# Performance work log

Hardware: AMD Instinct MI355X
Metric: run time of the kernel (lower is better)

Reference implementation:

```python
import jax, jax.numpy as jnp
import numpy as np

B, T, C = 2, 2048, 2048
N_HEAD = 16

def setup_inputs() -> dict:
    key = jax.random.key(0)
    k1, k2, k3 = jax.random.split(key, 3)
    scale = 1.0 / np.sqrt(C)
    return {
        "x": jax.random.normal(k1, (B, T, C), dtype=jnp.float32),
        "w_attn": jax.random.normal(k2, (C, 3 * C), dtype=jnp.float32) * scale,
        "b_attn": jnp.zeros((3 * C,), dtype=jnp.float32),
        "w_proj": jax.random.normal(k3, (C, C), dtype=jnp.float32) * scale,
        "b_proj": jnp.zeros((C,), dtype=jnp.float32),
    }

def reference(x, w_attn, b_attn, w_proj, b_proj):
    Bb, Tt, Cc = x.shape
    hd = Cc // N_HEAD  # head_size
    qkv = x @ w_attn + b_attn              # [B,T,3C]
    q, k, v = jnp.split(qkv, 3, axis=-1)
    # [B,T,C] -> [B,H,T,hd]
    def heads(t):
        return t.reshape(Bb, Tt, N_HEAD, hd).transpose(0, 2, 1, 3)
    q, k, v = heads(q), heads(k), heads(v)
    att = jnp.einsum("bhqd,bhkd->bhqk", q, k) * (hd ** -0.5)
    causal = jnp.tril(jnp.ones((Tt, Tt), dtype=bool))
    att = jnp.where(causal[None, None], att, -jnp.inf)
    att = jax.nn.softmax(att, axis=-1)
    out = jnp.einsum("bhqk,bhkd->bhqd", att, v)
    out = out.transpose(0, 2, 1, 3).reshape(Bb, Tt, Cc)
    return out @ w_proj + b_proj
```

## Files before the change

kernel.cpp:

```cpp
#include <hip/hip_runtime.h>
#include <cstdint>
#include <cstddef>

typedef __bf16 bf16_t;
typedef __bf16 bf16x8 __attribute__((ext_vector_type(8)));
typedef __bf16 bf16x4 __attribute__((ext_vector_type(4)));
typedef float floatx4 __attribute__((ext_vector_type(4)));

#define B_  2
#define T_  2048
#define C_  2048
#define H_  16
#define HD_ 128

#define K_ATTN_SCALE (0.08838834764831843f * 1.44269504088896f)

__device__ __forceinline__ void async_copy16(const void* g, void* l) {
  __builtin_amdgcn_global_load_lds((const __attribute__((address_space(1))) unsigned int*)g,
                                   (__attribute__((address_space(3))) unsigned int*)l,
                                   16, 0, 0);
}

__global__ __launch_bounds__(256) void cvt_f32_bf16(const float* __restrict__ in,
                                                    bf16_t* __restrict__ out, int n4) {
  int i = blockIdx.x * 256 + threadIdx.x;
  if (i >= n4) return;
  const float4 v = ((const float4*)in)[i];
  bf16x4 o;
  o[0] = (bf16_t)v.x; o[1] = (bf16_t)v.y; o[2] = (bf16_t)v.z; o[3] = (bf16_t)v.w;
  ((bf16x4*)out)[i] = o;
}

__global__ __launch_bounds__(256) void transpose_cvt(const float* __restrict__ W,
                                                     bf16_t* __restrict__ Wt,
                                                     int Kd, int Nd) {
  __shared__ float tile[32][33];
  const int tx = threadIdx.x, ty = threadIdx.y;
  const int n0 = blockIdx.x * 32, k0 = blockIdx.y * 32;
#pragma unroll
  for (int j = ty; j < 32; j += 8)
    tile[j][tx] = W[(size_t)(k0 + j) * Nd + n0 + tx];
  __syncthreads();
#pragma unroll
  for (int j = ty; j < 32; j += 8)
    Wt[(size_t)(n0 + j) * Kd + k0 + tx] = (bf16_t)tile[tx][j];
}

#define TM 128
#define TN 128
#define BK 64

template <int MODE>
__global__ __launch_bounds__(256) void gemm_bt(
    const bf16_t* __restrict__ A, const bf16_t* __restrict__ Bt,
    const float* __restrict__ bias, float* __restrict__ Cout,
    bf16_t* __restrict__ Qo, bf16_t* __restrict__ Ko, bf16_t* __restrict__ Vo,
    int M, int N, int K) {
  __shared__ __align__(16) char smem[32768];
  bf16_t (*As)[BK] = (bf16_t(*)[BK])smem;
  bf16_t (*Bs)[BK] = (bf16_t(*)[BK])(smem + 16384);
  const int tid = threadIdx.x;
  const int wave = tid >> 6, lane = tid & 63;
  const int quad = lane >> 4, l15 = lane & 15;
  const int bm = blockIdx.y * TM, bn = blockIdx.x * TN;
  const int wm = (wave >> 1) * 64, wn = (wave & 1) * 64;
  const int sw = l15 & 7;

  floatx4 acc[4][4] = {};

  for (int k0 = 0; k0 < K; k0 += BK) {
#pragma unroll
    for (int it = 0; it < 4; ++it) {
      int p = it * 4096 + tid * 16;
      int r = p >> 7;
      int cg = ((p >> 4) & 7) ^ (r & 7);
      async_copy16(A + (size_t)(bm + r) * K + k0 + cg * 8, (char*)&As[0][0] + p);
      async_copy16(Bt + (size_t)(bn + r) * K + k0 + cg * 8, (char*)&Bs[0][0] + p);
    }
    __syncthreads();
#pragma unroll
    for (int kc = 0; kc < 2; ++kc) {
      const int cidx = (kc * 4 + quad) ^ sw;
      bf16x8 af[4], bf[4];
#pragma unroll
      for (int i = 0; i < 4; ++i)
        af[i] = *(const bf16x8*)&As[wm + i * 16 + l15][cidx * 8];
#pragma unroll
      for (int j = 0; j < 4; ++j)
        bf[j] = *(const bf16x8*)&Bs[wn + j * 16 + l15][cidx * 8];
#pragma unroll
      for (int i = 0; i < 4; ++i)
#pragma unroll
        for (int j = 0; j < 4; ++j)
          acc[i][j] = __builtin_amdgcn_mfma_f32_16x16x32_bf16(af[i], bf[j], acc[i][j], 0, 0, 0);
    }
    __syncthreads();
  }

  if (MODE == 0 && bn >= 2 * C_) {
    bf16_t* vt = (bf16_t*)smem;
    const int h = (bn - 2 * C_) >> 7;
    const int b = bm >> 11;
    const int t0g = bm & 2047;
#pragma unroll
    for (int i = 0; i < 4; ++i) {
#pragma unroll
      for (int j = 0; j < 4; ++j) {
#pragma unroll
        for (int r = 0; r < 4; ++r) {
          int tl = wm + i * 16 + quad * 4 + r;
          int d  = wn + j * 16 + l15;
          float val = acc[i][j][r] + bias[bn + wn + j * 16 + l15];
          vt[d * 128 + (tl ^ (8 * (d & 15)))] = (bf16_t)val;
        }
      }
    }
    __syncthreads();
    const int row = tid >> 1, half = tid & 1;
    bf16_t* dst = Vo + ((size_t)(b * H_ + h) * HD_ + row) * T_ + t0g;
#pragma unroll
    for (int cc = 0; cc < 8; ++cc) {
      int c = half * 8 + cc;
      uint4 v = *(const uint4*)&vt[row * 128 + ((c ^ (row & 15)) * 8)];
      *(uint4*)(dst + c * 8) = v;
    }
    return;
  }

#pragma unroll
  for (int i = 0; i < 4; ++i) {
#pragma unroll
    for (int j = 0; j < 4; ++j) {
#pragma unroll
      for (int r = 0; r < 4; ++r) {
        int m = bm + wm + i * 16 + quad * 4 + r;
        int n = bn + wn + j * 16 + l15;
        float val = acc[i][j][r] + bias[n];
        if (MODE == 1) {
          Cout[(size_t)m * N + n] = val;
        } else {
          int which = n >> 11;
          int cc = n & 2047;
          int h = cc >> 7, d = cc & 127;
          int b = m >> 11, t = m & 2047;
          if (which == 0) val *= K_ATTN_SCALE;
          bf16_t bv = (bf16_t)val;
          bf16_t* dst = (which == 0) ? Qo : Ko;
          dst[(((size_t)(b * H_ + h)) * T_ + t) * HD_ + d] = bv;
        }
      }
    }
  }
}

__global__ __launch_bounds__(256) void attn(const bf16_t* __restrict__ Q,
                                            const bf16_t* __restrict__ Kg,
                                            const bf16_t* __restrict__ Vt,
                                            bf16_t* __restrict__ O) {
  __shared__ bf16_t Ks[2][64][128];
  __shared__ bf16_t Vs[2][128][64];
  const int tid = threadIdx.x;
  const int wave = tid >> 6, lane = tid & 63;
  const int quad = lane >> 4, l15 = lane & 15;
  const int j = blockIdx.x;
  const int bh = blockIdx.y;
  const int b = bh >> 4, h = bh & 15;
  const int qtA = 31 - j, qtB = j;
  const int nchA = qtA + 1, nchB = qtB + 1;
  const int q0A = qtA * 64 + wave * 16;
  const int q0B = qtB * 64 + wave * 16;

  const bf16_t* Qh = Q + (size_t)bh * T_ * HD_;
  const bf16_t* Kh = Kg + (size_t)bh * T_ * HD_;
  const bf16_t* Vh = Vt + (size_t)bh * HD_ * T_;

  bf16x8 qfA[4], qfB[4];
#pragma unroll
  for (int kk = 0; kk < 4; ++kk) {
    qfA[kk] = *(const bf16x8*)(Qh + (size_t)(q0A + l15) * HD_ + kk * 32 + quad * 8);
    qfB[kk] = *(const bf16x8*)(Qh + (size_t)(q0B + l15) * HD_ + kk * 32 + quad * 8);
  }

  floatx4 oaccA[8] = {}, oaccB[8] = {};
  float l_A = 0.0f, l_B = 0.0f;

  union PU { bf16x4 v; long long u; };
  union PF { long long u[2]; bf16x8 v; };
  const int lo = ((lane & 16) << 1) + l15;

  auto stage = [&](int buf, int kt0) {
#pragma unroll
    for (int it = 0; it < 4; ++it) {
      int p = it * 4096 + tid * 16;
      int r = p >> 8;
      int cg = ((p >> 4) & 15) ^ (r & 15);
      async_copy16(Kh + (size_t)(kt0 + r) * HD_ + cg * 8, (char*)&Ks[buf][0][0] + p);
    }
#pragma unroll
    for (int it = 0; it < 4; ++it) {
      int p = it * 4096 + tid * 16;
      int r = p >> 7;
      int cg = ((p >> 4) & 7) ^ (r & 7);
      async_copy16(Vh + (size_t)r * T_ + kt0 + cg * 8, (char*)&Vs[buf][0][0] + p);
    }
  };

  auto step = [&](int buf, const bf16x8* qf, floatx4* oacc, float& l_i, int q0, int kt0,
                  bool mask) {
    floatx4 s[4] = {{}, {}, {}, {}};
#pragma unroll
    for (int st = 0; st < 4; ++st) {
#pragma unroll
      for (int kk = 0; kk < 4; ++kk) {
        bf16x8 kf = *(const bf16x8*)&Ks[buf][st * 16 + l15][(((kk * 4 + quad) ^ l15) & 15) * 8];
        s[st] = __builtin_amdgcn_mfma_f32_16x16x32_bf16(kf, qf[kk], s[st], 0, 0, 0);
      }
    }
    float ps = 0.0f;
    long long pu[4];
#pragma unroll
    for (int st = 0; st < 4; ++st) {
      PU t;
#pragma unroll
      for (int r = 0; r < 4; ++r) {
        float val = s[st][r];
        if (mask) {
          int kt = kt0 + st * 16 + quad * 4 + r;
          val = (kt <= q0 + l15) ? val : -3.0e38f;
        }
        float p = exp2f(val);
        ps += p;
        t.v[r] = (bf16_t)p;
      }
      pu[st] = t.u;
    }
    ps += __shfl_xor(ps, 16);
    ps += __shfl_xor(ps, 32);
    l_i += ps;
#pragma unroll
    for (int bb = 0; bb < 2; ++bb) {
      long long lo0 = __shfl(pu[2 * bb], lo);
      long long hi0 = __shfl(pu[2 * bb], lo + 16);
      long long lo1 = __shfl(pu[2 * bb + 1], lo);
      long long hi1 = __shfl(pu[2 * bb + 1], lo + 16);
      PF pf;
      pf.u[0] = (quad >= 2) ? lo1 : lo0;
      pf.u[1] = (quad >= 2) ? hi1 : hi0;
#pragma unroll
      for (int dt = 0; dt < 8; ++dt) {
        bf16x8 vf = *(const bf16x8*)&Vs[buf][dt * 16 + l15][(((bb * 4 + quad) ^ l15) & 7) * 8];
        oacc[dt] = __builtin_amdgcn_mfma_f32_16x16x32_bf16(pf.v, vf, oacc[dt], 0, 0, 0);
      }
    }
  };

  stage(0, 0);
  for (int ch = 0; ch < nchA; ++ch) {
    __syncthreads();
    if (ch + 1 < nchA) stage((ch + 1) & 1, (ch + 1) * 64);
    const int kt0 = ch * 64;
    const int buf = ch & 1;
    step(buf, qfA, oaccA, l_A, q0A, kt0, ch == nchA - 1);
    if (ch < nchB) step(buf, qfB, oaccB, l_B, q0B, kt0, ch == nchB - 1);
  }

  float lrA[4], lrB[4];
#pragma unroll
  for (int r = 0; r < 4; ++r) {
    lrA[r] = __shfl(l_A, quad * 4 + r);
    lrB[r] = __shfl(l_B, quad * 4 + r);
  }
#pragma unroll
  for (int dt = 0; dt < 8; ++dt) {
#pragma unroll
    for (int r = 0; r < 4; ++r) {
      int d = dt * 16 + l15;
      int qa = q0A + quad * 4 + r;
      int qb = q0B + quad * 4 + r;
      O[((size_t)(b * T_ + qa)) * C_ + h * HD_ + d] = (bf16_t)(oaccA[dt][r] / lrA[r]);
      O[((size_t)(b * T_ + qb)) * C_ + h * HD_ + d] = (bf16_t)(oaccB[dt][r] / lrB[r]);
    }
  }
}

extern "C" void kernel_launch(void* const* d_in, const int* in_sizes, int n_in,
                              void* d_out, int out_size, void* d_ws, size_t ws_size,
                              hipStream_t stream) {
  const float* x      = (const float*)d_in[0];
  const float* w_attn = (const float*)d_in[1];
  const float* b_attn = (const float*)d_in[2];
  const float* w_proj = (const float*)d_in[3];
  const float* b_proj = (const float*)d_in[4];
  float* out = (float*)d_out;

  char* p = (char*)d_ws;
  bf16_t* xb  = (bf16_t*)p; p += (size_t)4096 * 2048 * 2;
  bf16_t* waT = (bf16_t*)p; p += (size_t)6144 * 2048 * 2;
  bf16_t* wpT = (bf16_t*)p; p += (size_t)2048 * 2048 * 2;
  bf16_t* Qb  = (bf16_t*)p; p += (size_t)32 * 2048 * 128 * 2;
  bf16_t* Kb  = (bf16_t*)p; p += (size_t)32 * 2048 * 128 * 2;
  bf16_t* Vb  = (bf16_t*)p; p += (size_t)32 * 2048 * 128 * 2;
  bf16_t* Ob  = (bf16_t*)p; p += (size_t)4096 * 2048 * 2;

  cvt_f32_bf16<<<8192, 256, 0, stream>>>(x, xb, 2097152);
  transpose_cvt<<<dim3(6144 / 32, 2048 / 32), dim3(32, 8), 0, stream>>>(w_attn, waT, 2048, 6144);
  transpose_cvt<<<dim3(2048 / 32, 2048 / 32), dim3(32, 8), 0, stream>>>(w_proj, wpT, 2048, 2048);

  gemm_bt<0><<<dim3(6144 / TN, 4096 / TM), 256, 0, stream>>>(
      xb, waT, b_attn, nullptr, Qb, Kb, Vb, 4096, 6144, 2048);

  attn<<<dim3(16, 32), 256, 0, stream>>>(Qb, Kb, Vb, Ob);

  gemm_bt<1><<<dim3(2048 / TN, 4096 / TM), 256, 0, stream>>>(
      Ob, wpT, b_proj, out, nullptr, nullptr, nullptr, 4096, 2048, 2048);
}
```

Measured before the change: 421.0 us.

## Split attention to one query tile per block, read V from global, narrow proj GEMM tile

The attention kernel stops pairing two query tiles per block and launches one block per query tile, doubling the grid to 1024 blocks. It drops the V shared-memory staging in favour of direct global loads, and adds an occupancy hint of 4 blocks per CU. The output projection GEMM is templated to use a 64-wide N tile, doubling its block count to fill more CUs. The risks are uneven causal work per block with heaviest tiles first, uncoalesced V reads that lean on cache, and less operand reuse in the narrower GEMM tile.

```diff
diff --git a/kernel.cpp b/kernel.cpp
--- a/kernel.cpp
+++ b/kernel.cpp
@@ -47,26 +47,28 @@
 }
 
 #define TM 128
-#define TN 128
 #define BK 64
 
-template <int MODE>
+template <int MODE, int TNP>
 __global__ __launch_bounds__(256) void gemm_bt(
     const bf16_t* __restrict__ A, const bf16_t* __restrict__ Bt,
     const float* __restrict__ bias, float* __restrict__ Cout,
     bf16_t* __restrict__ Qo, bf16_t* __restrict__ Ko, bf16_t* __restrict__ Vo,
     int M, int N, int K) {
-  __shared__ __align__(16) char smem[32768];
+  constexpr int WN = (TNP == 128) ? 64 : 32;
+  constexpr int JN = WN / 16;
+  constexpr int BROUNDS = TNP * BK * 2 / 4096;
+  __shared__ __align__(16) char smem[(TM + TNP) * BK * 2];
   bf16_t (*As)[BK] = (bf16_t(*)[BK])smem;
-  bf16_t (*Bs)[BK] = (bf16_t(*)[BK])(smem + 16384);
+  bf16_t (*Bs)[BK] = (bf16_t(*)[BK])(smem + TM * BK * 2);
   const int tid = threadIdx.x;
   const int wave = tid >> 6, lane = tid & 63;
   const int quad = lane >> 4, l15 = lane & 15;
-  const int bm = blockIdx.y * TM, bn = blockIdx.x * TN;
-  const int wm = (wave >> 1) * 64, wn = (wave & 1) * 64;
+  const int bm = blockIdx.y * TM, bn = blockIdx.x * TNP;
+  const int wm = (wave >> 1) * 64, wn = (wave & 1) * WN;
   const int sw = l15 & 7;
 
-  floatx4 acc[4][4] = {};
+  floatx4 acc[4][JN] = {};
 
   for (int k0 = 0; k0 < K; k0 += BK) {
 #pragma unroll
@@ -75,23 +77,29 @@
       int r = p >> 7;
       int cg = ((p >> 4) & 7) ^ (r & 7);
       async_copy16(A + (size_t)(bm + r) * K + k0 + cg * 8, (char*)&As[0][0] + p);
+    }
+#pragma unroll
+    for (int it = 0; it < BROUNDS; ++it) {
+      int p = it * 4096 + tid * 16;
+      int r = p >> 7;
+      int cg = ((p >> 4) & 7) ^ (r & 7);
       async_copy16(Bt + (size_t)(bn + r) * K + k0 + cg * 8, (char*)&Bs[0][0] + p);
     }
     __syncthreads();
 #pragma unroll
     for (int kc = 0; kc < 2; ++kc) {
       const int cidx = (kc * 4 + quad) ^ sw;
-      bf16x8 af[4], bf[4];
+      bf16x8 af[4], bf[JN];
 #pragma unroll
       for (int i = 0; i < 4; ++i)
         af[i] = *(const bf16x8*)&As[wm + i * 16 + l15][cidx * 8];
 #pragma unroll
-      for (int j = 0; j < 4; ++j)
+      for (int j = 0; j < JN; ++j)
         bf[j] = *(const bf16x8*)&Bs[wn + j * 16 + l15][cidx * 8];
 #pragma unroll
       for (int i = 0; i < 4; ++i)
 #pragma unroll
-        for (int j = 0; j < 4; ++j)
+        for (int j = 0; j < JN; ++j)
           acc[i][j] = __builtin_amdgcn_mfma_f32_16x16x32_bf16(af[i], bf[j], acc[i][j], 0, 0, 0);
     }
     __syncthreads();
@@ -105,7 +113,7 @@
 #pragma unroll
     for (int i = 0; i < 4; ++i) {
 #pragma unroll
-      for (int j = 0; j < 4; ++j) {
+      for (int j = 0; j < JN; ++j) {
 #pragma unroll
         for (int r = 0; r < 4; ++r) {
           int tl = wm + i * 16 + quad * 4 + r;
@@ -130,7 +138,7 @@
 #pragma unroll
   for (int i = 0; i < 4; ++i) {
 #pragma unroll
-    for (int j = 0; j < 4; ++j) {
+    for (int j = 0; j < JN; ++j) {
 #pragma unroll
       for (int r = 0; r < 4; ++r) {
         int m = bm + wm + i * 16 + quad * 4 + r;
@@ -153,42 +161,37 @@
   }
 }
 
-__global__ __launch_bounds__(256) void attn(const bf16_t* __restrict__ Q,
-                                            const bf16_t* __restrict__ Kg,
-                                            const bf16_t* __restrict__ Vt,
-                                            bf16_t* __restrict__ O) {
+__global__ __launch_bounds__(256, 4) void attn(const bf16_t* __restrict__ Q,
+                                               const bf16_t* __restrict__ Kg,
+                                               const bf16_t* __restrict__ Vt,
+                                               bf16_t* __restrict__ O) {
   __shared__ bf16_t Ks[2][64][128];
-  __shared__ bf16_t Vs[2][128][64];
   const int tid = threadIdx.x;
   const int wave = tid >> 6, lane = tid & 63;
   const int quad = lane >> 4, l15 = lane & 15;
-  const int j = blockIdx.x;
+  const int qt = 31 - blockIdx.x;
   const int bh = blockIdx.y;
   const int b = bh >> 4, h = bh & 15;
-  const int qtA = 31 - j, qtB = j;
-  const int nchA = qtA + 1, nchB = qtB + 1;
-  const int q0A = qtA * 64 + wave * 16;
-  const int q0B = qtB * 64 + wave * 16;
+  const int q0 = qt * 64 + wave * 16;
+  const int nch = qt + 1;
 
   const bf16_t* Qh = Q + (size_t)bh * T_ * HD_;
   const bf16_t* Kh = Kg + (size_t)bh * T_ * HD_;
   const bf16_t* Vh = Vt + (size_t)bh * HD_ * T_;
 
-  bf16x8 qfA[4], qfB[4];
-#pragma unroll
-  for (int kk = 0; kk < 4; ++kk) {
-    qfA[kk] = *(const bf16x8*)(Qh + (size_t)(q0A + l15) * HD_ + kk * 32 + quad * 8);
-    qfB[kk] = *(const bf16x8*)(Qh + (size_t)(q0B + l15) * HD_ + kk * 32 + quad * 8);
-  }
-
-  floatx4 oaccA[8] = {}, oaccB[8] = {};
-  float l_A = 0.0f, l_B = 0.0f;
+  bf16x8 qf[4];
+#pragma unroll
+  for (int kk = 0; kk < 4; ++kk)
+    qf[kk] = *(const bf16x8*)(Qh + (size_t)(q0 + l15) * HD_ + kk * 32 + quad * 8);
+
+  floatx4 oacc[8] = {};
+  float l_i = 0.0f;
 
   union PU { bf16x4 v; long long u; };
   union PF { long long u[2]; bf16x8 v; };
   const int lo = ((lane & 16) << 1) + l15;
 
-  auto stage = [&](int buf, int kt0) {
+  auto stageK = [&](int buf, int kt0) {
 #pragma unroll
     for (int it = 0; it < 4; ++it) {
       int p = it * 4096 + tid * 16;
@@ -196,17 +199,16 @@
       int cg = ((p >> 4) & 15) ^ (r & 15);
       async_copy16(Kh + (size_t)(kt0 + r) * HD_ + cg * 8, (char*)&Ks[buf][0][0] + p);
     }
-#pragma unroll
-    for (int it = 0; it < 4; ++it) {
-      int p = it * 4096 + tid * 16;
-      int r = p >> 7;
-      int cg = ((p >> 4) & 7) ^ (r & 7);
-      async_copy16(Vh + (size_t)r * T_ + kt0 + cg * 8, (char*)&Vs[buf][0][0] + p);
-    }
   };
 
-  auto step = [&](int buf, const bf16x8* qf, floatx4* oacc, float& l_i, int q0, int kt0,
-                  bool mask) {
+  stageK(0, 0);
+  for (int ch = 0; ch < nch; ++ch) {
+    __syncthreads();
+    if (ch + 1 < nch) stageK((ch + 1) & 1, (ch + 1) * 64);
+    const int kt0 = ch * 64;
+    const int buf = ch & 1;
+    const bool mask = (ch == nch - 1);
+
     floatx4 s[4] = {{}, {}, {}, {}};
 #pragma unroll
     for (int st = 0; st < 4; ++st) {
@@ -216,6 +218,7 @@
         s[st] = __builtin_amdgcn_mfma_f32_16x16x32_bf16(kf, qf[kk], s[st], 0, 0, 0);
       }
     }
+
     float ps = 0.0f;
     long long pu[4];
 #pragma unroll
@@ -237,6 +240,7 @@
     ps += __shfl_xor(ps, 16);
     ps += __shfl_xor(ps, 32);
     l_i += ps;
+
 #pragma unroll
     for (int bb = 0; bb < 2; ++bb) {
       long long lo0 = __shfl(pu[2 * bb], lo);
@@ -246,39 +250,25 @@
       PF pf;
       pf.u[0] = (quad >= 2) ? lo1 : lo0;
       pf.u[1] = (quad >= 2) ? hi1 : hi0;
+      const bf16_t* vbase = Vh + (size_t)l15 * T_ + kt0 + bb * 32 + quad * 8;
 #pragma unroll
       for (int dt = 0; dt < 8; ++dt) {
-        bf16x8 vf = *(const bf16x8*)&Vs[buf][dt * 16 + l15][(((bb * 4 + quad) ^ l15) & 7) * 8];
+        bf16x8 vf = *(const bf16x8*)(vbase + (size_t)dt * 16 * T_);
         oacc[dt] = __builtin_amdgcn_mfma_f32_16x16x32_bf16(pf.v, vf, oacc[dt], 0, 0, 0);
       }
     }
-  };
-
-  stage(0, 0);
-  for (int ch = 0; ch < nchA; ++ch) {
-    __syncthreads();
-    if (ch + 1 < nchA) stage((ch + 1) & 1, (ch + 1) * 64);
-    const int kt0 = ch * 64;
-    const int buf = ch & 1;
-    step(buf, qfA, oaccA, l_A, q0A, kt0, ch == nchA - 1);
-    if (ch < nchB) step(buf, qfB, oaccB, l_B, q0B, kt0, ch == nchB - 1);
-  }
-
-  float lrA[4], lrB[4];
-#pragma unroll
-  for (int r = 0; r < 4; ++r) {
-    lrA[r] = __shfl(l_A, quad * 4 + r);
-    lrB[r] = __shfl(l_B, quad * 4 + r);
-  }
+  }
+
+  float lr[4];
+#pragma unroll
+  for (int r = 0; r < 4; ++r) lr[r] = __shfl(l_i, quad * 4 + r);
 #pragma unroll
   for (int dt = 0; dt < 8; ++dt) {
 #pragma unroll
     for (int r = 0; r < 4; ++r) {
       int d = dt * 16 + l15;
-      int qa = q0A + quad * 4 + r;
-      int qb = q0B + quad * 4 + r;
-      O[((size_t)(b * T_ + qa)) * C_ + h * HD_ + d] = (bf16_t)(oaccA[dt][r] / lrA[r]);
-      O[((size_t)(b * T_ + qb)) * C_ + h * HD_ + d] = (bf16_t)(oaccB[dt][r] / lrB[r]);
+      int qq = q0 + quad * 4 + r;
+      O[((size_t)(b * T_ + qq)) * C_ + h * HD_ + d] = (bf16_t)(oacc[dt][r] / lr[r]);
     }
   }
 }
@@ -306,11 +296,11 @@
   transpose_cvt<<<dim3(6144 / 32, 2048 / 32), dim3(32, 8), 0, stream>>>(w_attn, waT, 2048, 6144);
   transpose_cvt<<<dim3(2048 / 32, 2048 / 32), dim3(32, 8), 0, stream>>>(w_proj, wpT, 2048, 2048);
 
-  gemm_bt<0><<<dim3(6144 / TN, 4096 / TM), 256, 0, stream>>>(
+  gemm_bt<0, 128><<<dim3(6144 / 128, 4096 / TM), 256, 0, stream>>>(
       xb, waT, b_attn, nullptr, Qb, Kb, Vb, 4096, 6144, 2048);
 
-  attn<<<dim3(16, 32), 256, 0, stream>>>(Qb, Kb, Vb, Ob);
-
-  gemm_bt<1><<<dim3(2048 / TN, 4096 / TM), 256, 0, stream>>>(
+  attn<<<dim3(32, 32), 256, 0, stream>>>(Qb, Kb, Vb, Ob);
+
+  gemm_bt<1, 64><<<dim3(2048 / 64, 4096 / TM), 256, 0, stream>>>(
       Ob, wpT, b_proj, out, nullptr, nullptr, nullptr, 4096, 2048, 2048);
 }
```

New measurement: 557.0 us. +32.3%, slower.
